# Performance work log

Hardware: AMD Instinct MI355X
Metric: run time of the kernel (lower is better)

## Reference

```python
import jax, jax.numpy as jnp
import numpy as np

N = 50000
E = 800000
D = 256
C = 4
BN_EPS = 1e-5


def setup_inputs() -> dict:
    key = jax.random.key(0)
    ks = jax.random.split(key, 12)
    x = jax.random.normal(ks[0], (N, D), dtype=jnp.float32)
    edge_index = jax.random.randint(ks[1], (2, E), 0, N)
    edge_attr = jax.random.normal(ks[2], (E, D), dtype=jnp.float32)
    # cluster partition -> one-hot masks [C, N]
    assign = jax.random.randint(ks[3], (N,), 0, C)
    masks = jax.nn.one_hot(assign, C, dtype=jnp.float32).T  # [C, N]
    complement_masks = 1.0 - masks
    # per-cluster GINEConv MLP params (2-layer MLP), eps, and BN affine params
    s = 1.0 / np.sqrt(D)
    W1 = jax.random.uniform(ks[4], (C, D, D), jnp.float32, -s, s)
    b1 = jnp.zeros((C, D), jnp.float32)
    W2 = jax.random.uniform(ks[5], (C, D, D), jnp.float32, -s, s)
    b2 = jnp.zeros((C, D), jnp.float32)
    eps = jnp.zeros((C,), jnp.float32)        # train_eps init 0
    gamma = jnp.ones((C, D), jnp.float32)
    beta = jnp.zeros((C, D), jnp.float32)
    return {"x": x, "edge_index": edge_index, "edge_attr": edge_attr,
            "masks": masks, "complement_masks": complement_masks,
            "W1": W1, "b1": b1, "W2": W2, "b2": b2,
            "eps": eps, "gamma": gamma, "beta": beta}


def _gine_conv(x, src, dst, edge_attr, W1, b1, W2, b2, eps):
    # message: ReLU(x_j + e_ij), sum-aggregate at target i
    msg = jax.nn.relu(x[src] + edge_attr)            # [E, D]
    aggr = jax.ops.segment_sum(msg, dst, num_segments=N)  # [N, D]
    h = (1.0 + eps) * x + aggr
    h = jax.nn.relu(h @ W1 + b1) @ W2 + b2
    return h


def _batch_norm(x, gamma, beta):
    mean = jnp.mean(x, axis=0)
    var = jnp.mean((x - mean) ** 2, axis=0)  # biased, as in BN forward
    return gamma * (x - mean) * jax.lax.rsqrt(var + BN_EPS) + beta


def reference(x, edge_index, edge_attr, masks, complement_masks,
              W1, b1, W2, b2, eps, gamma, beta):
    src, dst = edge_index[0], edge_index[1]
    x_in = x
    for c in range(C):
        x_tmp = x
        h = _gine_conv(x, src, dst, edge_attr, W1[c], b1[c], W2[c], b2[c], eps[c])
        # sublayer_residual: masked update + full residual
        x = masks[c][:, None] * h + x_tmp
        x = _batch_norm(x, gamma[c], beta[c])
    x = jax.nn.relu(x)  # dropout p=0.0 -> identity
    x = x_in + x        # residual
    return x
```

## Files before the change

kernel.cpp:

```cpp
#include <hip/hip_runtime.h>

#define NN 50000
#define EE 800000
#define DD 256
#define CC 4
#define BN_EPSF 1e-5f
#define MROWS 48
#define ZPAD 268

typedef float v4f __attribute__((ext_vector_type(4)));
typedef float f32x4 __attribute__((ext_vector_type(4)));
typedef __bf16 bf16x8 __attribute__((ext_vector_type(8)));
typedef _Float16 h4 __attribute__((ext_vector_type(4)));


__global__ void k_hist(const int* __restrict__ dst, int* __restrict__ cnt) {
  int e = blockIdx.x * 256 + threadIdx.x;
  if (e < EE) atomicAdd(&cnt[dst[e]], 1);
}

__global__ void k_scan(int* __restrict__ cnt, int* __restrict__ rp) {
  __shared__ int wsums[16];
  __shared__ int sh_carry;
  __shared__ int sh_ctot;
  const int t = threadIdx.x;
  const int lane = t & 63;
  const int w = t >> 6;
  if (t == 0) sh_carry = 0;
  __syncthreads();
  for (int base = 0; base < NN; base += 1024) {
    int i = base + t;
    int v = (i < NN) ? cnt[i] : 0;
    int incl = v;
#pragma unroll
    for (int off = 1; off < 64; off <<= 1) {
      int u = __shfl_up(incl, off, 64);
      if (lane >= off) incl += u;
    }
    if (lane == 63) wsums[w] = incl;
    int cbase = sh_carry;
    __syncthreads();
    if (w == 0) {
      int s = (lane < 16) ? wsums[lane] : 0;
      int si = s;
#pragma unroll
      for (int off = 1; off < 16; off <<= 1) {
        int u = __shfl_up(si, off, 64);
        if (lane >= off) si += u;
      }
      if (lane < 16) wsums[lane] = si - s;
      if (lane == 15) sh_ctot = si;
    }
    __syncthreads();
    int excl = cbase + wsums[w] + (incl - v);
    if (i < NN) { rp[i] = excl; cnt[i] = excl; }
    __syncthreads();
    if (t == 0) sh_carry = cbase + sh_ctot;
    __syncthreads();
  }
  if (t == 0) rp[NN] = sh_carry;
}

__global__ void k_scatter(const int* __restrict__ src, const int* __restrict__ dst,
                          int* __restrict__ cur, int2* __restrict__ sse) {
  int e = blockIdx.x * 256 + threadIdx.x;
  if (e < EE) {
    int d = dst[e];
    int p = atomicAdd(&cur[d], 1);
    sse[p] = make_int2(src[e], e);
  }
}

__global__ void k_compact(const float* __restrict__ masks, int* __restrict__ ncount,
                          int* __restrict__ nlist, int* __restrict__ pcl) {
  int i = blockIdx.x * 256 + threadIdx.x;
  if (i >= NN) return;
  int c = 0;
#pragma unroll
  for (int k = 1; k < CC; ++k)
    if (masks[(size_t)k * NN + i] > 0.5f) c = k;
  int li = atomicAdd(&ncount[c], 1);
  nlist[c * NN + li] = i;
  pcl[i] = (c << 28) | li;
}

__global__ void k_wfmt(const float* __restrict__ W1, const float* __restrict__ W2,
                       __bf16* __restrict__ wf) {
  int b = blockIdx.x;
  int c = b >> 4, mat = (b >> 3) & 1, kk = b & 7;
  const float* W = (mat ? W2 : W1) + (size_t)c * DD * DD;
  __bf16* base = wf + (size_t)(c * 2 + mat) * 2 * 65536;
  int t = threadIdx.x;
  int lane = t & 63, cq = t >> 6;
  int l4 = lane >> 4, l16 = lane & 15;
#pragma unroll
  for (int ci = 0; ci < 4; ++ci) {
    int cg = cq * 4 + ci;
    bf16x8 hi, lo;
#pragma unroll
    for (int j = 0; j < 8; ++j) {
      float v = W[(size_t)(kk * 32 + l4 * 8 + j) * DD + cg * 16 + l16];
      __bf16 h = (__bf16)v;
      hi[j] = h;
      lo[j] = (__bf16)(v - (float)h);
    }
    size_t off = ((size_t)(kk * 16 + cg) * 64 + lane) * 8;
    *(bf16x8*)(base + off) = hi;
    *(bf16x8*)(base + 65536 + off) = lo;
  }
}


__device__ __forceinline__ v4f relu4(v4f s) {
  s.x = fmaxf(s.x, 0.f); s.y = fmaxf(s.y, 0.f);
  s.z = fmaxf(s.z, 0.f); s.w = fmaxf(s.w, 0.f);
  return s;
}

__global__ __launch_bounds__(256) void k_prep(const float* __restrict__ xin,
                                              _Float16* __restrict__ x16,
                                              float* __restrict__ g1,
                                              float* __restrict__ g2) {
  __shared__ float s1[DD], s2[DD];
  const int t = threadIdx.x;
  s1[t] = 0.f;
  s2[t] = 0.f;
  float ps[4] = {0.f, 0.f, 0.f, 0.f};
  float pq[4] = {0.f, 0.f, 0.f, 0.f};
  const int stride = gridDim.x * 256;
  for (int idx = blockIdx.x * 256 + t; idx < NN * DD / 4; idx += stride) {
    float4 v = ((const float4*)xin)[idx];
    h4 o;
    o.x = (_Float16)v.x; o.y = (_Float16)v.y;
    o.z = (_Float16)v.z; o.w = (_Float16)v.w;
    ((h4*)x16)[idx] = o;
    ps[0] += v.x; ps[1] += v.y; ps[2] += v.z; ps[3] += v.w;
    pq[0] += v.x * v.x; pq[1] += v.y * v.y; pq[2] += v.z * v.z; pq[3] += v.w * v.w;
  }
  __syncthreads();
  const int c4 = (t & 63) << 2;
#pragma unroll
  for (int j = 0; j < 4; ++j) {
    atomicAdd(&s1[c4 + j], ps[j]);
    atomicAdd(&s2[c4 + j], pq[j]);
  }
  __syncthreads();
  atomicAdd(&g1[t], s1[t]);
  atomicAdd(&g2[t], s2[t]);
}

__global__ __launch_bounds__(256) void k_aggregate_m(
    const _Float16* __restrict__ x16, const float* __restrict__ ea,
    const int* __restrict__ rp, const int2* __restrict__ sse,
    const int* __restrict__ nlist_c, const int* __restrict__ ncnt_c,
    float* __restrict__ aggrc) {
  int li = (blockIdx.x * 256 + threadIdx.x) >> 6;
  int lane = threadIdx.x & 63;
  if (li >= *ncnt_c) return;
  int node = nlist_c[li];
  int beg = rp[node], end = rp[node + 1];
  v4f acc = {0.f, 0.f, 0.f, 0.f};
  int p = beg;
  for (; p + 4 <= end; p += 4) {
    int2 d0 = sse[p];
    int2 d1 = sse[p + 1];
    int2 d2 = sse[p + 2];
    int2 d3 = sse[p + 3];
    v4f a0 = __builtin_nontemporal_load(((const v4f*)(ea + (size_t)d0.y * DD)) + lane);
    v4f a1 = __builtin_nontemporal_load(((const v4f*)(ea + (size_t)d1.y * DD)) + lane);
    v4f a2 = __builtin_nontemporal_load(((const v4f*)(ea + (size_t)d2.y * DD)) + lane);
    v4f a3 = __builtin_nontemporal_load(((const v4f*)(ea + (size_t)d3.y * DD)) + lane);
    h4 x0 = ((const h4*)(x16 + (size_t)d0.x * DD))[lane];
    h4 x1 = ((const h4*)(x16 + (size_t)d1.x * DD))[lane];
    h4 x2 = ((const h4*)(x16 + (size_t)d2.x * DD))[lane];
    h4 x3 = ((const h4*)(x16 + (size_t)d3.x * DD))[lane];
    acc += relu4(__builtin_convertvector(x0, v4f) + a0);
    acc += relu4(__builtin_convertvector(x1, v4f) + a1);
    acc += relu4(__builtin_convertvector(x2, v4f) + a2);
    acc += relu4(__builtin_convertvector(x3, v4f) + a3);
  }
  for (; p < end; ++p) {
    int2 d0 = sse[p];
    v4f a0 = __builtin_nontemporal_load(((const v4f*)(ea + (size_t)d0.y * DD)) + lane);
    h4 x0 = ((const h4*)(x16 + (size_t)d0.x * DD))[lane];
    acc += relu4(__builtin_convertvector(x0, v4f) + a0);
  }
  ((v4f*)(aggrc + (size_t)li * DD))[lane] = acc;
}

__device__ __forceinline__ void gemm_frag(
    const float (*zb)[ZPAD], const __bf16* __restrict__ wf,
    const float* __restrict__ bias, f32x4 (&acc)[3][4], int w, int lane) {
  const int l4 = lane >> 4, l16 = lane & 15;
#pragma unroll
  for (int cg = 0; cg < 4; ++cg) {
    float bv = bias[w * 64 + cg * 16 + l16];
    f32x4 b4 = {bv, bv, bv, bv};
#pragma unroll
    for (int mg = 0; mg < 3; ++mg) acc[mg][cg] = b4;
  }
  for (int kk = 0; kk < 8; ++kk) {
    bf16x8 bh[4], bl[4];
#pragma unroll
    for (int cg = 0; cg < 4; ++cg) {
      const __bf16* p = wf + (((size_t)(kk * 16 + w * 4 + cg)) * 64 + lane) * 8;
      bh[cg] = *(const bf16x8*)p;
      bl[cg] = *(const bf16x8*)(p + 65536);
    }
#pragma unroll
    for (int mg = 0; mg < 3; ++mg) {
      const float* zp = &zb[mg * 16 + l16][kk * 32 + l4 * 8];
      float4 z0 = *(const float4*)zp;
      float4 z1 = *(const float4*)(zp + 4);
      float zv[8] = {z0.x, z0.y, z0.z, z0.w, z1.x, z1.y, z1.z, z1.w};
      bf16x8 ah, al;
#pragma unroll
      for (int j = 0; j < 8; ++j) {
        __bf16 h = (__bf16)zv[j];
        ah[j] = h;
        al[j] = (__bf16)(zv[j] - (float)h);
      }
#pragma unroll
      for (int cg = 0; cg < 4; ++cg) {
        acc[mg][cg] = __builtin_amdgcn_mfma_f32_16x16x32_bf16(al, bh[cg], acc[mg][cg], 0, 0, 0);
        acc[mg][cg] = __builtin_amdgcn_mfma_f32_16x16x32_bf16(ah, bl[cg], acc[mg][cg], 0, 0, 0);
        acc[mg][cg] = __builtin_amdgcn_mfma_f32_16x16x32_bf16(ah, bh[cg], acc[mg][cg], 0, 0, 0);
      }
    }
  }
}

__global__ __launch_bounds__(256, 2) void k_mlp_m(
    const float* __restrict__ xc, const float* __restrict__ aggrc,
    float* __restrict__ ycomp,
    const __bf16* __restrict__ wf1, const __bf16* __restrict__ wf2,
    const float* __restrict__ b1g, const float* __restrict__ b2g,
    const int* __restrict__ nlist_c, const int* __restrict__ ncnt_c,
    const float* __restrict__ epsp,
    float* __restrict__ gd1, float* __restrict__ gd2) {
  __shared__ __align__(16) float zbuf[MROWS][ZPAD];
  __shared__ float ssum[DD];
  __shared__ float ssq[DD];
  __shared__ int nls[MROWS];
  const int t = threadIdx.x;
  const int lane = t & 63, w = t >> 6;
  const int l4 = lane >> 4, l16 = lane & 15;
  const int ncnt = *ncnt_c;
  const int li0 = blockIdx.x * MROWS;
  if (li0 >= ncnt) return;
  if (t < MROWS) nls[t] = (li0 + t < ncnt) ? nlist_c[li0 + t] : -1;
  ssum[t] = 0.f;
  ssq[t] = 0.f;
  const float ep = 1.0f + epsp[0];
  __syncthreads();
#pragma unroll
  for (int i = 0; i < 12; ++i) {
    int f4 = t + 256 * i;
    int r = f4 >> 6, c4 = (f4 & 63) << 2;
    int nid = nls[r];
    float4 zv = make_float4(0.f, 0.f, 0.f, 0.f);
    if (nid >= 0) {
      float4 xv = *(const float4*)(xc + (size_t)nid * DD + c4);
      float4 av = *(const float4*)(aggrc + (size_t)(li0 + r) * DD + c4);
      zv.x = fmaf(ep, xv.x, av.x);
      zv.y = fmaf(ep, xv.y, av.y);
      zv.z = fmaf(ep, xv.z, av.z);
      zv.w = fmaf(ep, xv.w, av.w);
    }
    *(float4*)&zbuf[r][c4] = zv;
  }
  __syncthreads();
  f32x4 acc[3][4];
  gemm_frag(zbuf, wf1, b1g, acc, w, lane);
  __syncthreads();
#pragma unroll
  for (int mg = 0; mg < 3; ++mg)
#pragma unroll
    for (int cg = 0; cg < 4; ++cg)
#pragma unroll
      for (int r = 0; r < 4; ++r)
        zbuf[mg * 16 + l4 * 4 + r][w * 64 + cg * 16 + l16] = fmaxf(acc[mg][cg][r], 0.f);
  __syncthreads();
  f32x4 acc2[3][4];
  gemm_frag(zbuf, wf2, b2g, acc2, w, lane);
  float ps[4], pq[4];
#pragma unroll
  for (int cg = 0; cg < 4; ++cg) { ps[cg] = 0.f; pq[cg] = 0.f; }
#pragma unroll
  for (int mg = 0; mg < 3; ++mg) {
#pragma unroll
    for (int r = 0; r < 4; ++r) {
      int rb = mg * 16 + l4 * 4 + r;
      int nid = nls[rb];
      if (nid >= 0) {
#pragma unroll
        for (int cg = 0; cg < 4; ++cg) {
          int col = w * 64 + cg * 16 + l16;
          float xv = xc[(size_t)nid * DD + col];
          float hv = acc2[mg][cg][r];
          float yv = xv + hv;
          ycomp[(size_t)(li0 + rb) * DD + col] = yv;
          ps[cg] += hv;
          pq[cg] += yv * yv - xv * xv;
        }
      }
    }
  }
#pragma unroll
  for (int cg = 0; cg < 4; ++cg) {
    atomicAdd(&ssum[w * 64 + cg * 16 + l16], ps[cg]);
    atomicAdd(&ssq[w * 64 + cg * 16 + l16], pq[cg]);
  }
  __syncthreads();
  atomicAdd(&gd1[t], ssum[t]);
  atomicAdd(&gd2[t], ssq[t]);
}

__global__ void k_bnstats_m(const float* __restrict__ g1, const float* __restrict__ g2,
                            const float* __restrict__ gd1, const float* __restrict__ gd2,
                            const float* __restrict__ gamma_c, const float* __restrict__ beta_c,
                            float* __restrict__ scale, float* __restrict__ shift) {
  int d = threadIdx.x;
  const float inv_n = 1.0f / (float)NN;
  float mean = (g1[d] + gd1[d]) * inv_n;
  float var = fmaxf((g2[d] + gd2[d]) * inv_n - mean * mean, 0.f);
  float sc = gamma_c[d] * rsqrtf(var + BN_EPSF);
  scale[d] = sc;
  shift[d] = fmaf(-mean, sc, beta_c[d]);
}

__global__ __launch_bounds__(256) void k_bnapply(
    const float* __restrict__ xc, const float* __restrict__ ycomp,
    const int* __restrict__ pcl, const float* __restrict__ scale,
    const float* __restrict__ shift, float* __restrict__ xnew,
    _Float16* __restrict__ x16, float* __restrict__ g1, float* __restrict__ g2,
    const float* __restrict__ xin, float* __restrict__ outp,
    int cidx, int final) {
  __shared__ float s1[DD];
  __shared__ float s2[DD];
  const int t = threadIdx.x;
  const int lane = t & 63;
  s1[t] = 0.f;
  s2[t] = 0.f;
  v4f sc4 = ((const v4f*)scale)[lane];
  v4f sh4 = ((const v4f*)shift)[lane];
  float ps[4] = {0.f, 0.f, 0.f, 0.f};
  float pq[4] = {0.f, 0.f, 0.f, 0.f};
  const int wid0 = (blockIdx.x * 256 + t) >> 6;
  const int wstride = gridDim.x * 4;
  for (int i = wid0; i < NN; i += wstride) {
    v4f xv = ((const v4f*)(xc + (size_t)i * DD))[lane];
    int pc = pcl[i];
    v4f yv = xv;
    if ((pc >> 28) == cidx) {
      int li = pc & 0x0FFFFFFF;
      yv = ((const v4f*)(ycomp + (size_t)li * DD))[lane];
    }
    v4f xn = sc4 * yv + sh4;
    if (final) {
      v4f xi = ((const v4f*)(xin + (size_t)i * DD))[lane];
      v4f o = xi + relu4(xn);
      ((v4f*)(outp + (size_t)i * DD))[lane] = o;
    } else {
      ((v4f*)(xnew + (size_t)i * DD))[lane] = xn;
      h4 h;
      h.x = (_Float16)xn.x; h.y = (_Float16)xn.y;
      h.z = (_Float16)xn.z; h.w = (_Float16)xn.w;
      ((h4*)(x16 + (size_t)i * DD))[lane] = h;
      ps[0] += xn.x; ps[1] += xn.y; ps[2] += xn.z; ps[3] += xn.w;
      pq[0] += xn.x * xn.x; pq[1] += xn.y * xn.y;
      pq[2] += xn.z * xn.z; pq[3] += xn.w * xn.w;
    }
  }
  if (!final) {
    __syncthreads();
    const int c4 = lane << 2;
#pragma unroll
    for (int j = 0; j < 4; ++j) {
      atomicAdd(&s1[c4 + j], ps[j]);
      atomicAdd(&s2[c4 + j], pq[j]);
    }
    __syncthreads();
    atomicAdd(&g1[t], s1[t]);
    atomicAdd(&g2[t], s2[t]);
  }
}


extern "C" void kernel_launch(void* const* d_in, const int* in_sizes, int n_in,
                              void* d_out, int out_size, void* d_ws, size_t ws_size,
                              hipStream_t stream) {
  (void)in_sizes; (void)n_in; (void)out_size; (void)ws_size;
  const float* x_in  = (const float*)d_in[0];
  const int*   ei    = (const int*)d_in[1];
  const float* ea    = (const float*)d_in[2];
  const float* masks = (const float*)d_in[3];
  const float* W1    = (const float*)d_in[5];
  const float* b1    = (const float*)d_in[6];
  const float* W2    = (const float*)d_in[7];
  const float* b2    = (const float*)d_in[8];
  const float* eps   = (const float*)d_in[9];
  const float* gamma = (const float*)d_in[10];
  const float* beta  = (const float*)d_in[11];
  float* out = (float*)d_out;

  float* xcur  = (float*)d_ws;
  float* ycomp = xcur + (size_t)NN * DD;
  float* aggrc = ycomp + (size_t)NN * DD;
  _Float16* x16 = (_Float16*)(aggrc + (size_t)NN * DD);
  int2*  sse   = (int2*)(x16 + (size_t)NN * DD);
  int*   rp    = (int*)(sse + EE);
  int*   cnt   = rp + 50016;
  int*   nlist = cnt + 50016;
  int*   pcl   = nlist + CC * NN;
  int*   ncount = pcl + NN;
  float* gx1   = (float*)(ncount + 16);
  float* gx2   = gx1 + 5 * DD;
  float* gd1   = gx2 + 5 * DD;
  float* gd2   = gd1 + CC * DD;
  float* scale = gd2 + CC * DD;
  float* shift = scale + DD;
  __bf16* wfmt = (__bf16*)(shift + DD);

  const int* src = ei;
  const int* dst = ei + EE;

  hipMemsetAsync(cnt, 0, NN * sizeof(int), stream);
  hipMemsetAsync(ncount, 0, 16 * sizeof(int), stream);
  hipMemsetAsync(gx1, 0, (5 + 5 + CC + CC) * DD * sizeof(float), stream);

  k_wfmt<<<64, 256, 0, stream>>>(W1, W2, wfmt);
  k_hist<<<EE / 256, 256, 0, stream>>>(dst, cnt);
  k_scan<<<1, 1024, 0, stream>>>(cnt, rp);
  k_scatter<<<EE / 256, 256, 0, stream>>>(src, dst, cnt, sse);
  k_compact<<<(NN + 255) / 256, 256, 0, stream>>>(masks, ncount, nlist, pcl);
  k_prep<<<1024, 256, 0, stream>>>(x_in, x16, gx1, gx2);

  for (int c = 0; c < CC; ++c) {
    const float* xc = (c == 0) ? x_in : xcur;
    k_aggregate_m<<<(NN * 64 + 255) / 256, 256, 0, stream>>>(
        x16, ea, rp, sse, nlist + c * NN, ncount + c, aggrc);
    k_mlp_m<<<(NN + MROWS - 1) / MROWS, 256, 0, stream>>>(
        xc, aggrc, ycomp,
        wfmt + (size_t)(c * 2 + 0) * 2 * 65536,
        wfmt + (size_t)(c * 2 + 1) * 2 * 65536,
        b1 + (size_t)c * DD, b2 + (size_t)c * DD,
        nlist + c * NN, ncount + c, eps + c,
        gd1 + c * DD, gd2 + c * DD);
    k_bnstats_m<<<1, DD, 0, stream>>>(gx1 + c * DD, gx2 + c * DD,
                                      gd1 + c * DD, gd2 + c * DD,
                                      gamma + (size_t)c * DD, beta + (size_t)c * DD,
                                      scale, shift);
    k_bnapply<<<1024, 256, 0, stream>>>(
        xc, ycomp, pcl, scale, shift, xcur, x16,
        gx1 + (c + 1) * DD, gx2 + (c + 1) * DD,
        x_in, out, c, (c == CC - 1) ? 1 : 0);
  }
}
```

Before: 1.856 ms.

## Pre-permute edge features to fp16 in cluster-sorted CSR order, fuse BN stats

Edges are now ordered by cluster-local destination, and edge_attr is converted once to fp16 and written in CSR order. Per-cluster aggregation then streams contiguous half-precision edge rows instead of gathering fp32 rows by edge id, which roughly halves edge-feature traffic across the four cluster passes. The BN scale/shift computation is folded into the apply kernel, removing one tiny launch per cluster. In exchange there is a one-time pass reading all fp32 edge features and writing a permuted fp16 copy, extra workspace, and fp16 rounding of edge_attr.

```diff
diff --git a/kernel.cpp b/kernel.cpp
--- a/kernel.cpp
+++ b/kernel.cpp
@@ -14,9 +14,35 @@
 typedef _Float16 h4 __attribute__((ext_vector_type(4)));
 
 
-__global__ void k_hist(const int* __restrict__ dst, int* __restrict__ cnt) {
+__global__ void k_compact(const float* __restrict__ masks, int* __restrict__ ncount,
+                          int* __restrict__ nlist, int* __restrict__ pcl) {
+  int i = blockIdx.x * 256 + threadIdx.x;
+  if (i >= NN) return;
+  int c = 0;
+#pragma unroll
+  for (int k = 1; k < CC; ++k)
+    if (masks[(size_t)k * NN + i] > 0.5f) c = k;
+  int li = atomicAdd(&ncount[c], 1);
+  nlist[c * NN + li] = i;
+  pcl[i] = (c << 28) | li;
+}
+
+__global__ void k_bases(const int* __restrict__ ncount, int* __restrict__ base) {
+  if (threadIdx.x == 0) {
+    int b = 0;
+#pragma unroll
+    for (int c = 0; c < CC; ++c) { base[c] = b; b += ncount[c]; }
+  }
+}
+
+
+__global__ void k_hist(const int* __restrict__ dst, const int* __restrict__ pcl,
+                       const int* __restrict__ base, int* __restrict__ cnt) {
   int e = blockIdx.x * 256 + threadIdx.x;
-  if (e < EE) atomicAdd(&cnt[dst[e]], 1);
+  if (e < EE) {
+    int pc = pcl[dst[e]];
+    atomicAdd(&cnt[base[pc >> 28] + (pc & 0x0FFFFFFF)], 1);
+  }
 }
 
 __global__ void k_scan(int* __restrict__ cnt, int* __restrict__ rp) {
@@ -61,27 +87,29 @@
   if (t == 0) rp[NN] = sh_carry;
 }
 
-__global__ void k_scatter(const int* __restrict__ src, const int* __restrict__ dst,
-                          int* __restrict__ cur, int2* __restrict__ sse) {
-  int e = blockIdx.x * 256 + threadIdx.x;
-  if (e < EE) {
-    int d = dst[e];
-    int p = atomicAdd(&cur[d], 1);
-    sse[p] = make_int2(src[e], e);
-  }
-}
-
-__global__ void k_compact(const float* __restrict__ masks, int* __restrict__ ncount,
-                          int* __restrict__ nlist, int* __restrict__ pcl) {
-  int i = blockIdx.x * 256 + threadIdx.x;
-  if (i >= NN) return;
-  int c = 0;
-#pragma unroll
-  for (int k = 1; k < CC; ++k)
-    if (masks[(size_t)k * NN + i] > 0.5f) c = k;
-  int li = atomicAdd(&ncount[c], 1);
-  nlist[c * NN + li] = i;
-  pcl[i] = (c << 28) | li;
+__global__ __launch_bounds__(256) void k_scatter_permute(
+    const int* __restrict__ src, const int* __restrict__ dst,
+    const int* __restrict__ pcl, const int* __restrict__ base,
+    int* __restrict__ cur, int* __restrict__ ss,
+    const float* __restrict__ ea, _Float16* __restrict__ ea16) {
+  int e = (blockIdx.x * 256 + threadIdx.x) >> 6;
+  int lane = threadIdx.x & 63;
+  if (e >= EE) return;
+  int p = 0;
+  if (lane == 0) {
+    int pc = pcl[dst[e]];
+    int g = base[pc >> 28] + (pc & 0x0FFFFFFF);
+    p = atomicAdd(&cur[g], 1);
+    ss[p] = src[e];
+  }
+  p = __shfl(p, 0, 64);
+  v4f v = __builtin_nontemporal_load(((const v4f*)(ea + (size_t)e * DD)) + lane);
+  h4 h;
+  h.x = (_Float16)v.x;
+  h.y = (_Float16)v.y;
+  h.z = (_Float16)v.z;
+  h.w = (_Float16)v.w;
+  __builtin_nontemporal_store(h, ((h4*)(ea16 + (size_t)p * DD)) + lane);
 }
 
 __global__ void k_wfmt(const float* __restrict__ W1, const float* __restrict__ W2,
@@ -150,40 +178,37 @@
 }
 
 __global__ __launch_bounds__(256) void k_aggregate_m(
-    const _Float16* __restrict__ x16, const float* __restrict__ ea,
-    const int* __restrict__ rp, const int2* __restrict__ sse,
-    const int* __restrict__ nlist_c, const int* __restrict__ ncnt_c,
-    float* __restrict__ aggrc) {
+    const _Float16* __restrict__ x16, const _Float16* __restrict__ ea16,
+    const int* __restrict__ rp, const int* __restrict__ ss,
+    const int* __restrict__ basep, const int* __restrict__ ncount,
+    int cidx, float* __restrict__ aggrc) {
   int li = (blockIdx.x * 256 + threadIdx.x) >> 6;
   int lane = threadIdx.x & 63;
-  if (li >= *ncnt_c) return;
-  int node = nlist_c[li];
-  int beg = rp[node], end = rp[node + 1];
+  if (li >= ncount[cidx]) return;
+  int g = basep[cidx] + li;
+  int beg = rp[g], end = rp[g + 1];
   v4f acc = {0.f, 0.f, 0.f, 0.f};
   int p = beg;
   for (; p + 4 <= end; p += 4) {
-    int2 d0 = sse[p];
-    int2 d1 = sse[p + 1];
-    int2 d2 = sse[p + 2];
-    int2 d3 = sse[p + 3];
-    v4f a0 = __builtin_nontemporal_load(((const v4f*)(ea + (size_t)d0.y * DD)) + lane);
-    v4f a1 = __builtin_nontemporal_load(((const v4f*)(ea + (size_t)d1.y * DD)) + lane);
-    v4f a2 = __builtin_nontemporal_load(((const v4f*)(ea + (size_t)d2.y * DD)) + lane);
-    v4f a3 = __builtin_nontemporal_load(((const v4f*)(ea + (size_t)d3.y * DD)) + lane);
-    h4 x0 = ((const h4*)(x16 + (size_t)d0.x * DD))[lane];
-    h4 x1 = ((const h4*)(x16 + (size_t)d1.x * DD))[lane];
-    h4 x2 = ((const h4*)(x16 + (size_t)d2.x * DD))[lane];
-    h4 x3 = ((const h4*)(x16 + (size_t)d3.x * DD))[lane];
-    acc += relu4(__builtin_convertvector(x0, v4f) + a0);
-    acc += relu4(__builtin_convertvector(x1, v4f) + a1);
-    acc += relu4(__builtin_convertvector(x2, v4f) + a2);
-    acc += relu4(__builtin_convertvector(x3, v4f) + a3);
+    int s0 = ss[p], s1 = ss[p + 1], s2 = ss[p + 2], s3 = ss[p + 3];
+    h4 e0 = __builtin_nontemporal_load(((const h4*)(ea16 + (size_t)p * DD)) + lane);
+    h4 e1 = __builtin_nontemporal_load(((const h4*)(ea16 + (size_t)(p + 1) * DD)) + lane);
+    h4 e2 = __builtin_nontemporal_load(((const h4*)(ea16 + (size_t)(p + 2) * DD)) + lane);
+    h4 e3 = __builtin_nontemporal_load(((const h4*)(ea16 + (size_t)(p + 3) * DD)) + lane);
+    h4 x0 = ((const h4*)(x16 + (size_t)s0 * DD))[lane];
+    h4 x1 = ((const h4*)(x16 + (size_t)s1 * DD))[lane];
+    h4 x2 = ((const h4*)(x16 + (size_t)s2 * DD))[lane];
+    h4 x3 = ((const h4*)(x16 + (size_t)s3 * DD))[lane];
+    acc += relu4(__builtin_convertvector(x0, v4f) + __builtin_convertvector(e0, v4f));
+    acc += relu4(__builtin_convertvector(x1, v4f) + __builtin_convertvector(e1, v4f));
+    acc += relu4(__builtin_convertvector(x2, v4f) + __builtin_convertvector(e2, v4f));
+    acc += relu4(__builtin_convertvector(x3, v4f) + __builtin_convertvector(e3, v4f));
   }
   for (; p < end; ++p) {
-    int2 d0 = sse[p];
-    v4f a0 = __builtin_nontemporal_load(((const v4f*)(ea + (size_t)d0.y * DD)) + lane);
-    h4 x0 = ((const h4*)(x16 + (size_t)d0.x * DD))[lane];
-    acc += relu4(__builtin_convertvector(x0, v4f) + a0);
+    int s0 = ss[p];
+    h4 e0 = __builtin_nontemporal_load(((const h4*)(ea16 + (size_t)p * DD)) + lane);
+    h4 x0 = ((const h4*)(x16 + (size_t)s0 * DD))[lane];
+    acc += relu4(__builtin_convertvector(x0, v4f) + __builtin_convertvector(e0, v4f));
   }
   ((v4f*)(aggrc + (size_t)li * DD))[lane] = acc;
 }
@@ -316,24 +341,14 @@
   atomicAdd(&gd2[t], ssq[t]);
 }
 
-__global__ void k_bnstats_m(const float* __restrict__ g1, const float* __restrict__ g2,
-                            const float* __restrict__ gd1, const float* __restrict__ gd2,
-                            const float* __restrict__ gamma_c, const float* __restrict__ beta_c,
-                            float* __restrict__ scale, float* __restrict__ shift) {
-  int d = threadIdx.x;
-  const float inv_n = 1.0f / (float)NN;
-  float mean = (g1[d] + gd1[d]) * inv_n;
-  float var = fmaxf((g2[d] + gd2[d]) * inv_n - mean * mean, 0.f);
-  float sc = gamma_c[d] * rsqrtf(var + BN_EPSF);
-  scale[d] = sc;
-  shift[d] = fmaf(-mean, sc, beta_c[d]);
-}
-
 __global__ __launch_bounds__(256) void k_bnapply(
     const float* __restrict__ xc, const float* __restrict__ ycomp,
-    const int* __restrict__ pcl, const float* __restrict__ scale,
-    const float* __restrict__ shift, float* __restrict__ xnew,
-    _Float16* __restrict__ x16, float* __restrict__ g1, float* __restrict__ g2,
+    const int* __restrict__ pcl,
+    const float* __restrict__ g1c, const float* __restrict__ g2c,
+    const float* __restrict__ gd1c, const float* __restrict__ gd2c,
+    const float* __restrict__ gamma_c, const float* __restrict__ beta_c,
+    float* __restrict__ xnew, _Float16* __restrict__ x16,
+    float* __restrict__ g1n, float* __restrict__ g2n,
     const float* __restrict__ xin, float* __restrict__ outp,
     int cidx, int final) {
   __shared__ float s1[DD];
@@ -342,8 +357,17 @@
   const int lane = t & 63;
   s1[t] = 0.f;
   s2[t] = 0.f;
-  v4f sc4 = ((const v4f*)scale)[lane];
-  v4f sh4 = ((const v4f*)shift)[lane];
+  const float inv_n = 1.0f / (float)NN;
+  v4f sc4, sh4;
+#pragma unroll
+  for (int j = 0; j < 4; ++j) {
+    int d = (lane << 2) + j;
+    float mean = (g1c[d] + gd1c[d]) * inv_n;
+    float var = fmaxf((g2c[d] + gd2c[d]) * inv_n - mean * mean, 0.f);
+    float sc = gamma_c[d] * rsqrtf(var + BN_EPSF);
+    sc4[j] = sc;
+    sh4[j] = fmaf(-mean, sc, beta_c[d]);
+  }
   float ps[4] = {0.f, 0.f, 0.f, 0.f};
   float pq[4] = {0.f, 0.f, 0.f, 0.f};
   const int wid0 = (blockIdx.x * 256 + t) >> 6;
@@ -381,8 +405,8 @@
       atomicAdd(&s2[c4 + j], pq[j]);
     }
     __syncthreads();
-    atomicAdd(&g1[t], s1[t]);
-    atomicAdd(&g2[t], s2[t]);
+    atomicAdd(&g1n[t], s1[t]);
+    atomicAdd(&g2n[t], s2[t]);
   }
 }
 
@@ -408,38 +432,39 @@
   float* ycomp = xcur + (size_t)NN * DD;
   float* aggrc = ycomp + (size_t)NN * DD;
   _Float16* x16 = (_Float16*)(aggrc + (size_t)NN * DD);
-  int2*  sse   = (int2*)(x16 + (size_t)NN * DD);
-  int*   rp    = (int*)(sse + EE);
+  _Float16* ea16 = x16 + (size_t)NN * DD;
+  int*   ss    = (int*)(ea16 + (size_t)EE * DD);
+  int*   rp    = ss + EE;
   int*   cnt   = rp + 50016;
   int*   nlist = cnt + 50016;
   int*   pcl   = nlist + CC * NN;
   int*   ncount = pcl + NN;
-  float* gx1   = (float*)(ncount + 16);
+  int*   base  = ncount + 16;
+  float* gx1   = (float*)(base + 16);
   float* gx2   = gx1 + 5 * DD;
   float* gd1   = gx2 + 5 * DD;
   float* gd2   = gd1 + CC * DD;
-  float* scale = gd2 + CC * DD;
-  float* shift = scale + DD;
-  __bf16* wfmt = (__bf16*)(shift + DD);
+  __bf16* wfmt = (__bf16*)(gd2 + CC * DD);
 
   const int* src = ei;
   const int* dst = ei + EE;
 
   hipMemsetAsync(cnt, 0, NN * sizeof(int), stream);
-  hipMemsetAsync(ncount, 0, 16 * sizeof(int), stream);
+  hipMemsetAsync(ncount, 0, 32 * sizeof(int), stream);
   hipMemsetAsync(gx1, 0, (5 + 5 + CC + CC) * DD * sizeof(float), stream);
 
   k_wfmt<<<64, 256, 0, stream>>>(W1, W2, wfmt);
-  k_hist<<<EE / 256, 256, 0, stream>>>(dst, cnt);
+  k_compact<<<(NN + 255) / 256, 256, 0, stream>>>(masks, ncount, nlist, pcl);
+  k_bases<<<1, 64, 0, stream>>>(ncount, base);
+  k_hist<<<EE / 256, 256, 0, stream>>>(dst, pcl, base, cnt);
   k_scan<<<1, 1024, 0, stream>>>(cnt, rp);
-  k_scatter<<<EE / 256, 256, 0, stream>>>(src, dst, cnt, sse);
-  k_compact<<<(NN + 255) / 256, 256, 0, stream>>>(masks, ncount, nlist, pcl);
+  k_scatter_permute<<<EE / 4, 256, 0, stream>>>(src, dst, pcl, base, cnt, ss, ea, ea16);
   k_prep<<<1024, 256, 0, stream>>>(x_in, x16, gx1, gx2);
 
   for (int c = 0; c < CC; ++c) {
     const float* xc = (c == 0) ? x_in : xcur;
     k_aggregate_m<<<(NN * 64 + 255) / 256, 256, 0, stream>>>(
-        x16, ea, rp, sse, nlist + c * NN, ncount + c, aggrc);
+        x16, ea16, rp, ss, base, ncount, c, aggrc);
     k_mlp_m<<<(NN + MROWS - 1) / MROWS, 256, 0, stream>>>(
         xc, aggrc, ycomp,
         wfmt + (size_t)(c * 2 + 0) * 2 * 65536,
@@ -447,13 +472,11 @@
         b1 + (size_t)c * DD, b2 + (size_t)c * DD,
         nlist + c * NN, ncount + c, eps + c,
         gd1 + c * DD, gd2 + c * DD);
-    k_bnstats_m<<<1, DD, 0, stream>>>(gx1 + c * DD, gx2 + c * DD,
-                                      gd1 + c * DD, gd2 + c * DD,
-                                      gamma + (size_t)c * DD, beta + (size_t)c * DD,
-                                      scale, shift);
     k_bnapply<<<1024, 256, 0, stream>>>(
-        xc, ycomp, pcl, scale, shift, xcur, x16,
-        gx1 + (c + 1) * DD, gx2 + (c + 1) * DD,
+        xc, ycomp, pcl,
+        gx1 + c * DD, gx2 + c * DD, gd1 + c * DD, gd2 + c * DD,
+        gamma + (size_t)c * DD, beta + (size_t)c * DD,
+        xcur, x16, gx1 + (c + 1) * DD, gx2 + (c + 1) * DD,
         x_in, out, c, (c == CC - 1) ? 1 : 0);
   }
 }
```

After: 2.118 ms. 14.1% more time.

## Fold batch-norm into lazy per-cluster affine transforms, dropping per-layer apply pass

Applied to the files above, without the earlier changes.

Removes the full-array BN apply kernel after each cluster layer. Each node's current value is kept as a stored base plus a per-cluster, per-channel affine (A, B) that accumulates successive BN scales and shifts. Statistics come analytically from per-cluster sums, and the affine is applied on the fly during aggregation, in the MLP input stage and in one final kernel. CSR rows are also reordered by cluster so each cluster's rows are contiguous. The cost is extra affine math and table selects in the gather loop, plus some numerical drift from computing variance via E[x^2]-mean^2 over composed affines.

```diff
diff --git a/kernel.cpp b/kernel.cpp
--- a/kernel.cpp
+++ b/kernel.cpp
@@ -14,9 +14,35 @@
 typedef _Float16 h4 __attribute__((ext_vector_type(4)));
 
 
-__global__ void k_hist(const int* __restrict__ dst, int* __restrict__ cnt) {
+__global__ void k_compact(const float* __restrict__ masks, int* __restrict__ ncount,
+                          int* __restrict__ nlist, int* __restrict__ pcl) {
+  int i = blockIdx.x * 256 + threadIdx.x;
+  if (i >= NN) return;
+  int c = 0;
+#pragma unroll
+  for (int k = 1; k < CC; ++k)
+    if (masks[(size_t)k * NN + i] > 0.5f) c = k;
+  int li = atomicAdd(&ncount[c], 1);
+  nlist[c * NN + li] = i;
+  pcl[i] = (c << 28) | li;
+}
+
+__global__ void k_bases(const int* __restrict__ ncount, int* __restrict__ base) {
+  if (threadIdx.x == 0) {
+    int b = 0;
+#pragma unroll
+    for (int c = 0; c < CC; ++c) { base[c] = b; b += ncount[c]; }
+  }
+}
+
+
+__global__ void k_hist(const int* __restrict__ dst, const int* __restrict__ pcl,
+                       const int* __restrict__ base, int* __restrict__ cnt) {
   int e = blockIdx.x * 256 + threadIdx.x;
-  if (e < EE) atomicAdd(&cnt[dst[e]], 1);
+  if (e < EE) {
+    int pc = pcl[dst[e]];
+    atomicAdd(&cnt[base[pc >> 28] + (pc & 0x0FFFFFFF)], 1);
+  }
 }
 
 __global__ void k_scan(int* __restrict__ cnt, int* __restrict__ rp) {
@@ -62,26 +88,17 @@
 }
 
 __global__ void k_scatter(const int* __restrict__ src, const int* __restrict__ dst,
+                          const int* __restrict__ pcl, const int* __restrict__ base,
                           int* __restrict__ cur, int2* __restrict__ sse) {
   int e = blockIdx.x * 256 + threadIdx.x;
   if (e < EE) {
-    int d = dst[e];
-    int p = atomicAdd(&cur[d], 1);
-    sse[p] = make_int2(src[e], e);
-  }
-}
-
-__global__ void k_compact(const float* __restrict__ masks, int* __restrict__ ncount,
-                          int* __restrict__ nlist, int* __restrict__ pcl) {
-  int i = blockIdx.x * 256 + threadIdx.x;
-  if (i >= NN) return;
-  int c = 0;
-#pragma unroll
-  for (int k = 1; k < CC; ++k)
-    if (masks[(size_t)k * NN + i] > 0.5f) c = k;
-  int li = atomicAdd(&ncount[c], 1);
-  nlist[c * NN + li] = i;
-  pcl[i] = (c << 28) | li;
+    int s = src[e];
+    int pcd = pcl[dst[e]];
+    int g = base[pcd >> 28] + (pcd & 0x0FFFFFFF);
+    int p = atomicAdd(&cur[g], 1);
+    int ms = ((unsigned)pcl[s]) >> 28;
+    sse[p] = make_int2((ms << 24) | s, e);
+  }
 }
 
 __global__ void k_wfmt(const float* __restrict__ W1, const float* __restrict__ W2,
@@ -117,48 +134,74 @@
   return s;
 }
 
-__global__ __launch_bounds__(256) void k_prep(const float* __restrict__ xin,
-                                              _Float16* __restrict__ x16,
-                                              float* __restrict__ g1,
-                                              float* __restrict__ g2) {
-  __shared__ float s1[DD], s2[DD];
+__global__ void k_init(float* __restrict__ Pg, float* __restrict__ Qg,
+                       float* __restrict__ tblA, float* __restrict__ tblB) {
+  int d = threadIdx.x;
+  Pg[d] = 1.f;
+  Qg[d] = 0.f;
+#pragma unroll
+  for (int m = 0; m < CC; ++m) {
+    tblA[m * DD + d] = 1.f;
+    tblB[m * DD + d] = 0.f;
+  }
+}
+
+__global__ __launch_bounds__(256) void k_prep(
+    const float* __restrict__ xin, const int* __restrict__ pcl,
+    _Float16* __restrict__ g16, float* __restrict__ s01, float* __restrict__ s02) {
+  __shared__ float s1[CC][DD];
+  __shared__ float s2[CC][DD];
   const int t = threadIdx.x;
-  s1[t] = 0.f;
-  s2[t] = 0.f;
-  float ps[4] = {0.f, 0.f, 0.f, 0.f};
-  float pq[4] = {0.f, 0.f, 0.f, 0.f};
-  const int stride = gridDim.x * 256;
-  for (int idx = blockIdx.x * 256 + t; idx < NN * DD / 4; idx += stride) {
-    float4 v = ((const float4*)xin)[idx];
-    h4 o;
-    o.x = (_Float16)v.x; o.y = (_Float16)v.y;
-    o.z = (_Float16)v.z; o.w = (_Float16)v.w;
-    ((h4*)x16)[idx] = o;
-    ps[0] += v.x; ps[1] += v.y; ps[2] += v.z; ps[3] += v.w;
-    pq[0] += v.x * v.x; pq[1] += v.y * v.y; pq[2] += v.z * v.z; pq[3] += v.w * v.w;
-  }
-  __syncthreads();
-  const int c4 = (t & 63) << 2;
-#pragma unroll
-  for (int j = 0; j < 4; ++j) {
-    atomicAdd(&s1[c4 + j], ps[j]);
-    atomicAdd(&s2[c4 + j], pq[j]);
-  }
-  __syncthreads();
-  atomicAdd(&g1[t], s1[t]);
-  atomicAdd(&g2[t], s2[t]);
+  const int lane = t & 63;
+#pragma unroll
+  for (int j = 0; j < CC; ++j) { s1[j][t] = 0.f; s2[j][t] = 0.f; }
+  __syncthreads();
+  const int c4 = lane << 2;
+  const int wid0 = (blockIdx.x * 256 + t) >> 6;
+  const int wstride = gridDim.x * 4;
+  for (int i = wid0; i < NN; i += wstride) {
+    int m = ((unsigned)pcl[i]) >> 28;
+    v4f xv = ((const v4f*)(xin + (size_t)i * DD))[lane];
+    h4 h;
+    h.x = (_Float16)xv.x; h.y = (_Float16)xv.y;
+    h.z = (_Float16)xv.z; h.w = (_Float16)xv.w;
+    ((h4*)(g16 + (size_t)i * DD))[lane] = h;
+    atomicAdd(&s1[m][c4 + 0], xv.x);
+    atomicAdd(&s1[m][c4 + 1], xv.y);
+    atomicAdd(&s1[m][c4 + 2], xv.z);
+    atomicAdd(&s1[m][c4 + 3], xv.w);
+    atomicAdd(&s2[m][c4 + 0], xv.x * xv.x);
+    atomicAdd(&s2[m][c4 + 1], xv.y * xv.y);
+    atomicAdd(&s2[m][c4 + 2], xv.z * xv.z);
+    atomicAdd(&s2[m][c4 + 3], xv.w * xv.w);
+  }
+  __syncthreads();
+#pragma unroll
+  for (int j = 0; j < CC; ++j) {
+    atomicAdd(&s01[j * DD + t], s1[j][t]);
+    atomicAdd(&s02[j * DD + t], s2[j][t]);
+  }
 }
 
 __global__ __launch_bounds__(256) void k_aggregate_m(
-    const _Float16* __restrict__ x16, const float* __restrict__ ea,
+    const _Float16* __restrict__ g16, const float* __restrict__ ea,
     const int* __restrict__ rp, const int2* __restrict__ sse,
-    const int* __restrict__ nlist_c, const int* __restrict__ ncnt_c,
-    float* __restrict__ aggrc) {
+    const int* __restrict__ basep, const int* __restrict__ ncount,
+    const float* __restrict__ tblA, const float* __restrict__ tblB,
+    int cidx, float* __restrict__ aggrc) {
   int li = (blockIdx.x * 256 + threadIdx.x) >> 6;
   int lane = threadIdx.x & 63;
-  if (li >= *ncnt_c) return;
-  int node = nlist_c[li];
-  int beg = rp[node], end = rp[node + 1];
+  if (li >= ncount[cidx]) return;
+  v4f A0 = ((const v4f*)(tblA + 0 * DD))[lane];
+  v4f A1 = ((const v4f*)(tblA + 1 * DD))[lane];
+  v4f A2 = ((const v4f*)(tblA + 2 * DD))[lane];
+  v4f A3 = ((const v4f*)(tblA + 3 * DD))[lane];
+  v4f B0 = ((const v4f*)(tblB + 0 * DD))[lane];
+  v4f B1 = ((const v4f*)(tblB + 1 * DD))[lane];
+  v4f B2 = ((const v4f*)(tblB + 2 * DD))[lane];
+  v4f B3 = ((const v4f*)(tblB + 3 * DD))[lane];
+  int g = basep[cidx] + li;
+  int beg = rp[g], end = rp[g + 1];
   v4f acc = {0.f, 0.f, 0.f, 0.f};
   int p = beg;
   for (; p + 4 <= end; p += 4) {
@@ -170,20 +213,33 @@
     v4f a1 = __builtin_nontemporal_load(((const v4f*)(ea + (size_t)d1.y * DD)) + lane);
     v4f a2 = __builtin_nontemporal_load(((const v4f*)(ea + (size_t)d2.y * DD)) + lane);
     v4f a3 = __builtin_nontemporal_load(((const v4f*)(ea + (size_t)d3.y * DD)) + lane);
-    h4 x0 = ((const h4*)(x16 + (size_t)d0.x * DD))[lane];
-    h4 x1 = ((const h4*)(x16 + (size_t)d1.x * DD))[lane];
-    h4 x2 = ((const h4*)(x16 + (size_t)d2.x * DD))[lane];
-    h4 x3 = ((const h4*)(x16 + (size_t)d3.x * DD))[lane];
-    acc += relu4(__builtin_convertvector(x0, v4f) + a0);
-    acc += relu4(__builtin_convertvector(x1, v4f) + a1);
-    acc += relu4(__builtin_convertvector(x2, v4f) + a2);
-    acc += relu4(__builtin_convertvector(x3, v4f) + a3);
+    h4 x0 = ((const h4*)(g16 + (size_t)(d0.x & 0x00FFFFFF) * DD))[lane];
+    h4 x1 = ((const h4*)(g16 + (size_t)(d1.x & 0x00FFFFFF) * DD))[lane];
+    h4 x2 = ((const h4*)(g16 + (size_t)(d2.x & 0x00FFFFFF) * DD))[lane];
+    h4 x3 = ((const h4*)(g16 + (size_t)(d3.x & 0x00FFFFFF) * DD))[lane];
+    int m0 = ((unsigned)d0.x) >> 24, m1 = ((unsigned)d1.x) >> 24;
+    int m2 = ((unsigned)d2.x) >> 24, m3 = ((unsigned)d3.x) >> 24;
+    v4f Aa = (m0 & 2) ? ((m0 & 1) ? A3 : A2) : ((m0 & 1) ? A1 : A0);
+    v4f Ba = (m0 & 2) ? ((m0 & 1) ? B3 : B2) : ((m0 & 1) ? B1 : B0);
+    acc += relu4(Aa * __builtin_convertvector(x0, v4f) + Ba + a0);
+    Aa = (m1 & 2) ? ((m1 & 1) ? A3 : A2) : ((m1 & 1) ? A1 : A0);
+    Ba = (m1 & 2) ? ((m1 & 1) ? B3 : B2) : ((m1 & 1) ? B1 : B0);
+    acc += relu4(Aa * __builtin_convertvector(x1, v4f) + Ba + a1);
+    Aa = (m2 & 2) ? ((m2 & 1) ? A3 : A2) : ((m2 & 1) ? A1 : A0);
+    Ba = (m2 & 2) ? ((m2 & 1) ? B3 : B2) : ((m2 & 1) ? B1 : B0);
+    acc += relu4(Aa * __builtin_convertvector(x2, v4f) + Ba + a2);
+    Aa = (m3 & 2) ? ((m3 & 1) ? A3 : A2) : ((m3 & 1) ? A1 : A0);
+    Ba = (m3 & 2) ? ((m3 & 1) ? B3 : B2) : ((m3 & 1) ? B1 : B0);
+    acc += relu4(Aa * __builtin_convertvector(x3, v4f) + Ba + a3);
   }
   for (; p < end; ++p) {
     int2 d0 = sse[p];
     v4f a0 = __builtin_nontemporal_load(((const v4f*)(ea + (size_t)d0.y * DD)) + lane);
-    h4 x0 = ((const h4*)(x16 + (size_t)d0.x * DD))[lane];
-    acc += relu4(__builtin_convertvector(x0, v4f) + a0);
+    h4 x0 = ((const h4*)(g16 + (size_t)(d0.x & 0x00FFFFFF) * DD))[lane];
+    int m0 = ((unsigned)d0.x) >> 24;
+    v4f Aa = (m0 & 2) ? ((m0 & 1) ? A3 : A2) : ((m0 & 1) ? A1 : A0);
+    v4f Ba = (m0 & 2) ? ((m0 & 1) ? B3 : B2) : ((m0 & 1) ? B1 : B0);
+    acc += relu4(Aa * __builtin_convertvector(x0, v4f) + Ba + a0);
   }
   ((v4f*)(aggrc + (size_t)li * DD))[lane] = acc;
 }
@@ -231,13 +287,14 @@
 }
 
 __global__ __launch_bounds__(256, 2) void k_mlp_m(
-    const float* __restrict__ xc, const float* __restrict__ aggrc,
-    float* __restrict__ ycomp,
+    const float* __restrict__ xin, const float* __restrict__ aggrc,
+    float* __restrict__ xbase, _Float16* __restrict__ g16,
     const __bf16* __restrict__ wf1, const __bf16* __restrict__ wf2,
     const float* __restrict__ b1g, const float* __restrict__ b2g,
     const int* __restrict__ nlist_c, const int* __restrict__ ncnt_c,
-    const float* __restrict__ epsp,
-    float* __restrict__ gd1, float* __restrict__ gd2) {
+    const float* __restrict__ epsp, const float* __restrict__ Pg,
+    const float* __restrict__ Qg,
+    float* __restrict__ sv1c, float* __restrict__ sv2c) {
   __shared__ __align__(16) float zbuf[MROWS][ZPAD];
   __shared__ float ssum[DD];
   __shared__ float ssq[DD];
@@ -253,21 +310,24 @@
   ssq[t] = 0.f;
   const float ep = 1.0f + epsp[0];
   __syncthreads();
+  const int c4s = (t & 63) << 2;
+  const float4 Pv4 = *(const float4*)(Pg + c4s);
+  const float4 Qv4 = *(const float4*)(Qg + c4s);
 #pragma unroll
   for (int i = 0; i < 12; ++i) {
     int f4 = t + 256 * i;
-    int r = f4 >> 6, c4 = (f4 & 63) << 2;
+    int r = f4 >> 6;
     int nid = nls[r];
     float4 zv = make_float4(0.f, 0.f, 0.f, 0.f);
     if (nid >= 0) {
-      float4 xv = *(const float4*)(xc + (size_t)nid * DD + c4);
-      float4 av = *(const float4*)(aggrc + (size_t)(li0 + r) * DD + c4);
-      zv.x = fmaf(ep, xv.x, av.x);
-      zv.y = fmaf(ep, xv.y, av.y);
-      zv.z = fmaf(ep, xv.z, av.z);
-      zv.w = fmaf(ep, xv.w, av.w);
-    }
-    *(float4*)&zbuf[r][c4] = zv;
+      float4 xv = *(const float4*)(xin + (size_t)nid * DD + c4s);
+      float4 av = *(const float4*)(aggrc + (size_t)(li0 + r) * DD + c4s);
+      zv.x = fmaf(ep, fmaf(Pv4.x, xv.x, Qv4.x), av.x);
+      zv.y = fmaf(ep, fmaf(Pv4.y, xv.y, Qv4.y), av.y);
+      zv.z = fmaf(ep, fmaf(Pv4.z, xv.z, Qv4.z), av.z);
+      zv.w = fmaf(ep, fmaf(Pv4.w, xv.w, Qv4.w), av.w);
+    }
+    *(float4*)&zbuf[r][c4s] = zv;
   }
   __syncthreads();
   f32x4 acc[3][4];
@@ -283,9 +343,15 @@
   __syncthreads();
   f32x4 acc2[3][4];
   gemm_frag(zbuf, wf2, b2g, acc2, w, lane);
-  float ps[4], pq[4];
-#pragma unroll
-  for (int cg = 0; cg < 4; ++cg) { ps[cg] = 0.f; pq[cg] = 0.f; }
+  float Pv[4], Qv[4], ps[4], pq[4];
+#pragma unroll
+  for (int cg = 0; cg < 4; ++cg) {
+    int col = w * 64 + cg * 16 + l16;
+    Pv[cg] = Pg[col];
+    Qv[cg] = Qg[col];
+    ps[cg] = 0.f;
+    pq[cg] = 0.f;
+  }
 #pragma unroll
   for (int mg = 0; mg < 3; ++mg) {
 #pragma unroll
@@ -296,12 +362,13 @@
 #pragma unroll
         for (int cg = 0; cg < 4; ++cg) {
           int col = w * 64 + cg * 16 + l16;
-          float xv = xc[(size_t)nid * DD + col];
-          float hv = acc2[mg][cg][r];
-          float yv = xv + hv;
-          ycomp[(size_t)(li0 + rb) * DD + col] = yv;
-          ps[cg] += hv;
-          pq[cg] += yv * yv - xv * xv;
+          float x0v = xin[(size_t)nid * DD + col];
+          float xcv = fmaf(Pv[cg], x0v, Qv[cg]);
+          float v = xcv + acc2[mg][cg][r];
+          xbase[(size_t)nid * DD + col] = v;
+          g16[(size_t)nid * DD + col] = (_Float16)v;
+          ps[cg] += v;
+          pq[cg] += v * v;
         }
       }
     }
@@ -312,77 +379,79 @@
     atomicAdd(&ssq[w * 64 + cg * 16 + l16], pq[cg]);
   }
   __syncthreads();
-  atomicAdd(&gd1[t], ssum[t]);
-  atomicAdd(&gd2[t], ssq[t]);
-}
-
-__global__ void k_bnstats_m(const float* __restrict__ g1, const float* __restrict__ g2,
-                            const float* __restrict__ gd1, const float* __restrict__ gd2,
-                            const float* __restrict__ gamma_c, const float* __restrict__ beta_c,
-                            float* __restrict__ scale, float* __restrict__ shift) {
+  atomicAdd(&sv1c[t], ssum[t]);
+  atomicAdd(&sv2c[t], ssq[t]);
+}
+
+__global__ void k_stats(const float* __restrict__ s01, const float* __restrict__ s02,
+                        const float* __restrict__ sv1, const float* __restrict__ sv2,
+                        const int* __restrict__ ncount,
+                        const float* __restrict__ gamma_c, const float* __restrict__ beta_c,
+                        float* __restrict__ Pg, float* __restrict__ Qg,
+                        float* __restrict__ Rg, float* __restrict__ Sg,
+                        float* __restrict__ tblA, float* __restrict__ tblB, int c) {
   int d = threadIdx.x;
+  float Pd = Pg[d], Qd = Qg[d];
+  float sum = 0.f, ssq = 0.f;
+#pragma unroll
+  for (int m = 0; m < CC; ++m) {
+    float n = (float)ncount[m];
+    if (m < c) {
+      float A = Rg[m * DD + d], B = Sg[m * DD + d];
+      sum += fmaf(A, sv1[m * DD + d], n * B);
+      ssq += A * A * sv2[m * DD + d] + 2.f * A * B * sv1[m * DD + d] + n * B * B;
+    } else if (m == c) {
+      sum += sv1[m * DD + d];
+      ssq += sv2[m * DD + d];
+    } else {
+      sum += fmaf(Pd, s01[m * DD + d], n * Qd);
+      ssq += Pd * Pd * s02[m * DD + d] + 2.f * Pd * Qd * s01[m * DD + d] + n * Qd * Qd;
+    }
+  }
   const float inv_n = 1.0f / (float)NN;
-  float mean = (g1[d] + gd1[d]) * inv_n;
-  float var = fmaxf((g2[d] + gd2[d]) * inv_n - mean * mean, 0.f);
+  float mean = sum * inv_n;
+  float var = fmaxf(ssq * inv_n - mean * mean, 0.f);
   float sc = gamma_c[d] * rsqrtf(var + BN_EPSF);
-  scale[d] = sc;
-  shift[d] = fmaf(-mean, sc, beta_c[d]);
-}
-
-__global__ __launch_bounds__(256) void k_bnapply(
-    const float* __restrict__ xc, const float* __restrict__ ycomp,
-    const int* __restrict__ pcl, const float* __restrict__ scale,
-    const float* __restrict__ shift, float* __restrict__ xnew,
-    _Float16* __restrict__ x16, float* __restrict__ g1, float* __restrict__ g2,
-    const float* __restrict__ xin, float* __restrict__ outp,
-    int cidx, int final) {
-  __shared__ float s1[DD];
-  __shared__ float s2[DD];
+  float sh = fmaf(-mean, sc, beta_c[d]);
+  float Pn = sc * Pd, Qn = fmaf(sc, Qd, sh);
+  Pg[d] = Pn;
+  Qg[d] = Qn;
+#pragma unroll
+  for (int m = 0; m < CC; ++m) {
+    if (m < c) {
+      float Rn = sc * Rg[m * DD + d];
+      float Sn = fmaf(sc, Sg[m * DD + d], sh);
+      Rg[m * DD + d] = Rn;
+      Sg[m * DD + d] = Sn;
+      tblA[m * DD + d] = Rn;
+      tblB[m * DD + d] = Sn;
+    } else if (m == c) {
+      Rg[m * DD + d] = sc;
+      Sg[m * DD + d] = sh;
+      tblA[m * DD + d] = sc;
+      tblB[m * DD + d] = sh;
+    } else {
+      tblA[m * DD + d] = Pn;
+      tblB[m * DD + d] = Qn;
+    }
+  }
+}
+
+__global__ __launch_bounds__(256) void k_final(
+    const float* __restrict__ xbase, const int* __restrict__ pcl,
+    const float* __restrict__ tblA, const float* __restrict__ tblB,
+    const float* __restrict__ xin, float* __restrict__ outp) {
   const int t = threadIdx.x;
   const int lane = t & 63;
-  s1[t] = 0.f;
-  s2[t] = 0.f;
-  v4f sc4 = ((const v4f*)scale)[lane];
-  v4f sh4 = ((const v4f*)shift)[lane];
-  float ps[4] = {0.f, 0.f, 0.f, 0.f};
-  float pq[4] = {0.f, 0.f, 0.f, 0.f};
   const int wid0 = (blockIdx.x * 256 + t) >> 6;
   const int wstride = gridDim.x * 4;
   for (int i = wid0; i < NN; i += wstride) {
-    v4f xv = ((const v4f*)(xc + (size_t)i * DD))[lane];
-    int pc = pcl[i];
-    v4f yv = xv;
-    if ((pc >> 28) == cidx) {
-      int li = pc & 0x0FFFFFFF;
-      yv = ((const v4f*)(ycomp + (size_t)li * DD))[lane];
-    }
-    v4f xn = sc4 * yv + sh4;
-    if (final) {
-      v4f xi = ((const v4f*)(xin + (size_t)i * DD))[lane];
-      v4f o = xi + relu4(xn);
-      ((v4f*)(outp + (size_t)i * DD))[lane] = o;
-    } else {
-      ((v4f*)(xnew + (size_t)i * DD))[lane] = xn;
-      h4 h;
-      h.x = (_Float16)xn.x; h.y = (_Float16)xn.y;
-      h.z = (_Float16)xn.z; h.w = (_Float16)xn.w;
-      ((h4*)(x16 + (size_t)i * DD))[lane] = h;
-      ps[0] += xn.x; ps[1] += xn.y; ps[2] += xn.z; ps[3] += xn.w;
-      pq[0] += xn.x * xn.x; pq[1] += xn.y * xn.y;
-      pq[2] += xn.z * xn.z; pq[3] += xn.w * xn.w;
-    }
-  }
-  if (!final) {
-    __syncthreads();
-    const int c4 = lane << 2;
-#pragma unroll
-    for (int j = 0; j < 4; ++j) {
-      atomicAdd(&s1[c4 + j], ps[j]);
-      atomicAdd(&s2[c4 + j], pq[j]);
-    }
-    __syncthreads();
-    atomicAdd(&g1[t], s1[t]);
-    atomicAdd(&g2[t], s2[t]);
+    int m = ((unsigned)pcl[i]) >> 28;
+    v4f v = ((const v4f*)(xbase + (size_t)i * DD))[lane];
+    v4f A = ((const v4f*)(tblA + (size_t)m * DD))[lane];
+    v4f B = ((const v4f*)(tblB + (size_t)m * DD))[lane];
+    v4f xi = ((const v4f*)(xin + (size_t)i * DD))[lane];
+    ((v4f*)(outp + (size_t)i * DD))[lane] = xi + relu4(A * v + B);
   }
 }
 
@@ -404,56 +473,57 @@
   const float* beta  = (const float*)d_in[11];
   float* out = (float*)d_out;
 
-  float* xcur  = (float*)d_ws;
-  float* ycomp = xcur + (size_t)NN * DD;
-  float* aggrc = ycomp + (size_t)NN * DD;
-  _Float16* x16 = (_Float16*)(aggrc + (size_t)NN * DD);
-  int2*  sse   = (int2*)(x16 + (size_t)NN * DD);
+  float* xbase = (float*)d_ws;
+  float* aggrc = xbase + (size_t)NN * DD;
+  _Float16* g16 = (_Float16*)(aggrc + (size_t)NN * DD);
+  int2*  sse   = (int2*)(g16 + (size_t)NN * DD);
   int*   rp    = (int*)(sse + EE);
   int*   cnt   = rp + 50016;
   int*   nlist = cnt + 50016;
   int*   pcl   = nlist + CC * NN;
   int*   ncount = pcl + NN;
-  float* gx1   = (float*)(ncount + 16);
-  float* gx2   = gx1 + 5 * DD;
-  float* gd1   = gx2 + 5 * DD;
-  float* gd2   = gd1 + CC * DD;
-  float* scale = gd2 + CC * DD;
-  float* shift = scale + DD;
-  __bf16* wfmt = (__bf16*)(shift + DD);
+  int*   base  = ncount + 16;
+  float* s01   = (float*)(base + 16);
+  float* s02   = s01 + CC * DD;
+  float* sv1   = s02 + CC * DD;
+  float* sv2   = sv1 + CC * DD;
+  float* Pg    = sv2 + CC * DD;
+  float* Qg    = Pg + DD;
+  float* Rg    = Qg + DD;
+  float* Sg    = Rg + CC * DD;
+  float* tblA  = Sg + CC * DD;
+  float* tblB  = tblA + CC * DD;
+  __bf16* wfmt = (__bf16*)(tblB + CC * DD);
 
   const int* src = ei;
   const int* dst = ei + EE;
 
   hipMemsetAsync(cnt, 0, NN * sizeof(int), stream);
-  hipMemsetAsync(ncount, 0, 16 * sizeof(int), stream);
-  hipMemsetAsync(gx1, 0, (5 + 5 + CC + CC) * DD * sizeof(float), stream);
+  hipMemsetAsync(ncount, 0, 32 * sizeof(int), stream);
+  hipMemsetAsync(s01, 0, 4 * CC * DD * sizeof(float), stream);
 
   k_wfmt<<<64, 256, 0, stream>>>(W1, W2, wfmt);
-  k_hist<<<EE / 256, 256, 0, stream>>>(dst, cnt);
+  k_compact<<<(NN + 255) / 256, 256, 0, stream>>>(masks, ncount, nlist, pcl);
+  k_bases<<<1, 64, 0, stream>>>(ncount, base);
+  k_hist<<<EE / 256, 256, 0, stream>>>(dst, pcl, base, cnt);
   k_scan<<<1, 1024, 0, stream>>>(cnt, rp);
-  k_scatter<<<EE / 256, 256, 0, stream>>>(src, dst, cnt, sse);
-  k_compact<<<(NN + 255) / 256, 256, 0, stream>>>(masks, ncount, nlist, pcl);
-  k_prep<<<1024, 256, 0, stream>>>(x_in, x16, gx1, gx2);
+  k_scatter<<<EE / 256, 256, 0, stream>>>(src, dst, pcl, base, cnt, sse);
+  k_init<<<1, DD, 0, stream>>>(Pg, Qg, tblA, tblB);
+  k_prep<<<256, 256, 0, stream>>>(x_in, pcl, g16, s01, s02);
 
   for (int c = 0; c < CC; ++c) {
-    const float* xc = (c == 0) ? x_in : xcur;
     k_aggregate_m<<<(NN * 64 + 255) / 256, 256, 0, stream>>>(
-        x16, ea, rp, sse, nlist + c * NN, ncount + c, aggrc);
+        g16, ea, rp, sse, base, ncount, tblA, tblB, c, aggrc);
     k_mlp_m<<<(NN + MROWS - 1) / MROWS, 256, 0, stream>>>(
-        xc, aggrc, ycomp,
+        x_in, aggrc, xbase, g16,
         wfmt + (size_t)(c * 2 + 0) * 2 * 65536,
         wfmt + (size_t)(c * 2 + 1) * 2 * 65536,
         b1 + (size_t)c * DD, b2 + (size_t)c * DD,
-        nlist + c * NN, ncount + c, eps + c,
-        gd1 + c * DD, gd2 + c * DD);
-    k_bnstats_m<<<1, DD, 0, stream>>>(gx1 + c * DD, gx2 + c * DD,
-                                      gd1 + c * DD, gd2 + c * DD,
-                                      gamma + (size_t)c * DD, beta + (size_t)c * DD,
-                                      scale, shift);
-    k_bnapply<<<1024, 256, 0, stream>>>(
-        xc, ycomp, pcl, scale, shift, xcur, x16,
-        gx1 + (c + 1) * DD, gx2 + (c + 1) * DD,
-        x_in, out, c, (c == CC - 1) ? 1 : 0);
-  }
-}
+        nlist + c * NN, ncount + c, eps + c, Pg, Qg,
+        sv1 + c * DD, sv2 + c * DD);
+    k_stats<<<1, DD, 0, stream>>>(s01, s02, sv1, sv2, ncount,
+                                  gamma + (size_t)c * DD, beta + (size_t)c * DD,
+                                  Pg, Qg, Rg, Sg, tblA, tblB, c);
+  }
+  k_final<<<512, 256, 0, stream>>>(xbase, pcl, tblA, tblB, x_in, out);
+}
```

New measurement: 1.845 ms. Within noise of the previous version (-0.6%).
